# Kernel optimization log

Measured on AMD Instinct MI355X. Metric: run time of the kernel, lower is better.

## Reference

```python
import jax, jax.numpy as jnp
import numpy as np
import math

NUM_HEADS = 16
D_MODEL = 1024
HEAD_DIM = D_MODEL // NUM_HEADS


def setup_inputs() -> dict:
    key = jax.random.key(0)
    k1, k2, k3 = jax.random.split(key, 3)
    x = jax.random.normal(k1, (4, 2048, D_MODEL), dtype=jnp.float32)
    # Linear(d_model, 3*d_model, bias=False): y = x @ w_qkv, w_qkv: [d_model, 3*d_model]
    w_qkv = jax.random.normal(k2, (D_MODEL, 3 * D_MODEL), dtype=jnp.float32) * (1.0 / math.sqrt(D_MODEL))
    w_o = jax.random.normal(k3, (D_MODEL, D_MODEL), dtype=jnp.float32) * (1.0 / math.sqrt(D_MODEL))
    return {"x": x, "w_qkv": w_qkv, "w_o": w_o}


def reference(x, w_qkv, w_o):
    B, S, _ = x.shape
    H, Dh = NUM_HEADS, HEAD_DIM
    qkv = (x @ w_qkv).reshape(B, S, 3, H, Dh)
    q = qkv[:, :, 0].transpose(0, 2, 1, 3)  # [B, H, S, Dh]
    k = qkv[:, :, 1].transpose(0, 2, 1, 3)
    v = qkv[:, :, 2].transpose(0, 2, 1, 3)
    scale = 1.0 / math.sqrt(Dh + 1e-9)
    scores = jnp.einsum("bhqd,bhkd->bhqk", q, k) * scale  # [B, H, S, S]
    probs = jax.nn.softmax(scores, axis=-1)
    # dropout is identity in eval mode
    out = jnp.einsum("bhqk,bhkd->bhqd", probs, v)  # [B, H, S, Dh]
    out = out.transpose(0, 2, 1, 3).reshape(B, S, H * Dh)
    return out @ w_o
```

## Files before the change

### kernel.cpp

```cpp
#include <hip/hip_runtime.h>
#include <hip/hip_bf16.h>

typedef __bf16 bf16_t;
typedef __bf16 bf16x8 __attribute__((ext_vector_type(8)));
typedef float f32x4 __attribute__((ext_vector_type(4)));
typedef unsigned int uint32x2 __attribute__((ext_vector_type(2)));
typedef unsigned int uint32x4 __attribute__((ext_vector_type(4)));

#define B_SZ 4
#define SEQ 2048
#define NH 16
#define DH 64
#define DM 1024
#define RSQ (3 * DM)

__device__ __forceinline__ void gload_lds16(const bf16_t* g, bf16_t* l) {
  __builtin_amdgcn_global_load_lds(
      (const __attribute__((address_space(1))) unsigned int*)g,
      (__attribute__((address_space(3))) unsigned int*)l, 16, 0, 0);
}

__device__ __forceinline__ unsigned lds_b32addr(void* p) {
  return (unsigned)(uintptr_t)(__attribute__((address_space(3))) void*)p;
}

__global__ __launch_bounds__(256) void f32_to_bf16_kernel(
    const float* __restrict__ in, bf16_t* __restrict__ out, int n) {
  int i = (blockIdx.x * blockDim.x + threadIdx.x) * 4;
  if (i >= n) return;
  float4 v = *reinterpret_cast<const float4*>(in + i);
  bf16_t o[4] = {(bf16_t)v.x, (bf16_t)v.y, (bf16_t)v.z, (bf16_t)v.w};
  *reinterpret_cast<uint2*>(out + i) = *reinterpret_cast<const uint2*>(o);
}

__global__ __launch_bounds__(256) void transpose_f32_bf16_kernel(
    const float* __restrict__ in, bf16_t* __restrict__ outT, int K, int N,
    int scale_cols, float scale) {
  __shared__ float tile[32][33];
  const int tx = threadIdx.x & 31;
  const int ty = threadIdx.x >> 5;
  const int n0 = blockIdx.x * 32;
  const int k0 = blockIdx.y * 32;
#pragma unroll
  for (int j = 0; j < 4; ++j)
    tile[ty + j * 8][tx] = in[(size_t)(k0 + ty + j * 8) * N + n0 + tx];
  __syncthreads();
#pragma unroll
  for (int j = 0; j < 4; ++j) {
    int n = n0 + ty + j * 8;
    float s = (n < scale_cols) ? scale : 1.0f;
    outT[(size_t)n * K + k0 + tx] = (bf16_t)(tile[tx][ty + j * 8] * s);
  }
}

template <typename OutT>
__global__ __launch_bounds__(512, 2) void gemm_dp_kernel(
    const bf16_t* __restrict__ A, const bf16_t* __restrict__ Bt,
    OutT* __restrict__ C, int M, int N, int K, int NB) {
  __shared__ __align__(16) bf16_t As[3][128 * 64];
  __shared__ __align__(16) bf16_t Bs[3][256 * 64];

  const int tid = threadIdx.x;
  const int lane = tid & 63;
  const int wid = tid >> 6;
  const int l16 = lane & 15;
  const int g4 = lane >> 4;
  const int wm = wid >> 2;
  const int wn = wid & 3;
  const int tiles = K >> 6;

  const int nwg = gridDim.x;
  const int bid = blockIdx.x;
  const int swz = (bid & 7) * (nwg >> 3) + (bid >> 3);
  const int m0 = (swz / NB) * 128;
  const int n0 = (swz % NB) * 256;

  const int srow = tid >> 3;
  const int scol = ((tid & 7) ^ (srow & 7)) * 8;
  const bf16_t* aglob = A + (size_t)(m0 + srow) * K + scol;
  const bf16_t* bglob = Bt + (size_t)(n0 + srow) * K + scol;

  auto stage = [&](int t) {
    const int buf = t % 3;
    const int k0 = t * 64;
#pragma unroll
    for (int i = 0; i < 2; ++i)
      gload_lds16(aglob + (size_t)i * 64 * K + k0,
                  &As[buf][i * 4096 + wid * 512]);
#pragma unroll
    for (int j = 0; j < 4; ++j)
      gload_lds16(bglob + (size_t)j * 64 * K + k0,
                  &Bs[buf][j * 4096 + wid * 512]);
  };

  f32x4 acc[4][4] = {};

  stage(0);
  stage(1);
  asm volatile("s_waitcnt vmcnt(6)" ::: "memory");
  __builtin_amdgcn_s_barrier();
  __builtin_amdgcn_sched_barrier(0);

  const int xr = l16 & 7;

  for (int t = 0; t < tiles; ++t) {
    const int buf = t % 3;

    bf16x8 af[4][2], bff[4][2];
#pragma unroll
    for (int m = 0; m < 4; ++m)
#pragma unroll
      for (int ks = 0; ks < 2; ++ks)
        af[m][ks] = *reinterpret_cast<const bf16x8*>(
            &As[buf][(wm * 64 + m * 16 + l16) * 64 +
                     ((ks * 4 + g4) ^ xr) * 8]);
#pragma unroll
    for (int n = 0; n < 4; ++n)
#pragma unroll
      for (int ks = 0; ks < 2; ++ks)
        bff[n][ks] = *reinterpret_cast<const bf16x8*>(
            &Bs[buf][(wn * 64 + n * 16 + l16) * 64 +
                     ((ks * 4 + g4) ^ xr) * 8]);

    if (t + 2 < tiles) stage(t + 2);

    __builtin_amdgcn_s_setprio(1);
#pragma unroll
    for (int m = 0; m < 4; ++m)
#pragma unroll
      for (int n = 0; n < 4; ++n)
#pragma unroll
        for (int ks = 0; ks < 2; ++ks)
          acc[m][n] = __builtin_amdgcn_mfma_f32_16x16x32_bf16(
              af[m][ks], bff[n][ks], acc[m][n], 0, 0, 0);
    __builtin_amdgcn_s_setprio(0);

    if (t + 2 < tiles)
      asm volatile("s_waitcnt vmcnt(6)" ::: "memory");
    else
      asm volatile("s_waitcnt vmcnt(0)" ::: "memory");
    __builtin_amdgcn_s_barrier();
    __builtin_amdgcn_sched_barrier(0);
  }

#pragma unroll
  for (int m = 0; m < 4; ++m)
#pragma unroll
    for (int n = 0; n < 4; ++n)
#pragma unroll
      for (int r = 0; r < 4; ++r) {
        int row = m0 + wm * 64 + m * 16 + g4 * 4 + r;
        int col = n0 + wn * 64 + n * 16 + l16;
        C[(size_t)row * N + col] = (OutT)acc[m][n][r];
      }
}

template <bool PRE>
__device__ __forceinline__ void attn_body(
    const bf16_t* kp_next, const bf16_t* vp_next, bf16_t* vst_next,
    unsigned vrd, uint32x4 (&kf)[2][2], const bf16x8 (&qf)[4][2],
    const bf16x8 vones, f32x4 (&acc_o)[16], f32x4 (&acc_l)[4]) {
  if constexpr (PRE) {
#pragma unroll
    for (int t = 0; t < 4; ++t)
      gload_lds16(vp_next + t * 16, vst_next + t * 512);
  }

  if constexpr (PRE)
    asm volatile("s_waitcnt vmcnt(8)" ::: "memory");
  else
    asm volatile("s_waitcnt vmcnt(4)" ::: "memory");
  __builtin_amdgcn_sched_barrier(0);

  uint32x2 vr[4][2];
#define TRR(dst, OFFSTR)                              \
  asm volatile("ds_read_b64_tr_b16 %0, %1 offset:" OFFSTR \
               : "=v"(dst)                            \
               : "v"(vrd))
  TRR(vr[0][0], "0");    TRR(vr[0][1], "512");
  TRR(vr[1][0], "1024"); TRR(vr[1][1], "1536");
  TRR(vr[2][0], "2048"); TRR(vr[2][1], "2560");
  TRR(vr[3][0], "3072"); TRR(vr[3][1], "3584");
#undef TRR

  if constexpr (PRE)
    asm volatile("s_waitcnt vmcnt(4)" ::: "memory");
  else
    asm volatile("s_waitcnt vmcnt(0)" ::: "memory");
  __builtin_amdgcn_sched_barrier(0);

  f32x4 sA[4] = {}, sB[4] = {};
#pragma unroll
  for (int qb = 0; qb < 4; ++qb) {
    sA[qb] = __builtin_amdgcn_mfma_f32_16x16x32_bf16(
        __builtin_bit_cast(bf16x8, kf[0][0]), qf[qb][0], sA[qb], 0, 0, 0);
    sA[qb] = __builtin_amdgcn_mfma_f32_16x16x32_bf16(
        __builtin_bit_cast(bf16x8, kf[0][1]), qf[qb][1], sA[qb], 0, 0, 0);
    sB[qb] = __builtin_amdgcn_mfma_f32_16x16x32_bf16(
        __builtin_bit_cast(bf16x8, kf[1][0]), qf[qb][0], sB[qb], 0, 0, 0);
    sB[qb] = __builtin_amdgcn_mfma_f32_16x16x32_bf16(
        __builtin_bit_cast(bf16x8, kf[1][1]), qf[qb][1], sB[qb], 0, 0, 0);
  }

  if constexpr (PRE) {
#pragma unroll
    for (int half = 0; half < 2; ++half)
#pragma unroll
      for (int kh = 0; kh < 2; ++kh)
        asm volatile("global_load_dwordx4 %0, %1, off"
                     : "=v"(kf[half][kh])
                     : "v"(kp_next + (size_t)half * 64 * RSQ + kh * 32)
                     : "memory");
  }

  const unsigned psel = 0x07060302u;
  bf16x8 pf[4];
#pragma unroll
  for (int qb = 0; qb < 4; ++qb) {
    unsigned b0 = __builtin_bit_cast(unsigned, __builtin_amdgcn_exp2f(sA[qb][0]));
    unsigned b1 = __builtin_bit_cast(unsigned, __builtin_amdgcn_exp2f(sA[qb][1]));
    unsigned b2 = __builtin_bit_cast(unsigned, __builtin_amdgcn_exp2f(sA[qb][2]));
    unsigned b3 = __builtin_bit_cast(unsigned, __builtin_amdgcn_exp2f(sA[qb][3]));
    unsigned b4 = __builtin_bit_cast(unsigned, __builtin_amdgcn_exp2f(sB[qb][0]));
    unsigned b5 = __builtin_bit_cast(unsigned, __builtin_amdgcn_exp2f(sB[qb][1]));
    unsigned b6 = __builtin_bit_cast(unsigned, __builtin_amdgcn_exp2f(sB[qb][2]));
    unsigned b7 = __builtin_bit_cast(unsigned, __builtin_amdgcn_exp2f(sB[qb][3]));
    unsigned u0, u1, u2, u3;
    asm("v_perm_b32 %0, %1, %2, %3" : "=v"(u0) : "v"(b1), "v"(b0), "v"(psel));
    asm("v_perm_b32 %0, %1, %2, %3" : "=v"(u1) : "v"(b3), "v"(b2), "v"(psel));
    asm("v_perm_b32 %0, %1, %2, %3" : "=v"(u2) : "v"(b5), "v"(b4), "v"(psel));
    asm("v_perm_b32 %0, %1, %2, %3" : "=v"(u3) : "v"(b7), "v"(b6), "v"(psel));
    uint32x4 pu = {u0, u1, u2, u3};
    pf[qb] = __builtin_bit_cast(bf16x8, pu);
  }

  asm volatile("s_waitcnt lgkmcnt(0)" ::: "memory");
  __builtin_amdgcn_sched_barrier(0);
  bf16x8 vf[4];
#pragma unroll
  for (int db = 0; db < 4; ++db) {
    uint32x4 c = {vr[db][0].x, vr[db][0].y, vr[db][1].x, vr[db][1].y};
    vf[db] = __builtin_bit_cast(bf16x8, c);
  }
#pragma unroll
  for (int qb = 0; qb < 4; ++qb) {
    acc_l[qb] = __builtin_amdgcn_mfma_f32_16x16x32_bf16(
        pf[qb], vones, acc_l[qb], 0, 0, 0);
#pragma unroll
    for (int db = 0; db < 4; ++db)
      acc_o[qb * 4 + db] = __builtin_amdgcn_mfma_f32_16x16x32_bf16(
          pf[qb], vf[db], acc_o[qb * 4 + db], 0, 0, 0);
  }
}

__global__ __launch_bounds__(256) void attn_kernel(
    const bf16_t* __restrict__ qkv, bf16_t* __restrict__ out) {
  __shared__ __align__(16) unsigned char smem[33792];
  bf16_t* Vlds = (bf16_t*)smem;
  float(*Obuf)[66] = (float(*)[66])smem;
  float* lbuf = (float*)(smem + 32768);

  const int tid = threadIdx.x;
  const int lane = tid & 63;
  const int wid = tid >> 6;
  const int l16 = lane & 15;
  const int g4 = lane >> 4;

  const int D = blockIdx.x;
  const int g = ((D >> 8) << 3) + (D & 7);
  const int h = g & 15;
  const int b = g >> 4;
  const int q0 = ((D >> 3) & 31) * 64;

  const size_t base = (size_t)b * SEQ * RSQ;

  bf16x8 qf[4][2];
#pragma unroll
  for (int qb = 0; qb < 4; ++qb)
#pragma unroll
    for (int kh = 0; kh < 2; ++kh)
      qf[qb][kh] = __builtin_bit_cast(
          bf16x8, *reinterpret_cast<const uint4*>(
                      qkv + base + (size_t)(q0 + qb * 16 + l16) * RSQ + h * DH +
                      kh * 32 + g4 * 8));

  const bf16_t* kbase =
      qkv + base + (size_t)(wid * 16 + l16) * RSQ + DM + h * DH + g4 * 8;

  const int keyoff = ((lane >> 5) << 6) + wid * 16 + (((lane >> 3) & 3) << 2) +
                     ((lane >> 1) & 3);
  const bf16_t* vsrc =
      qkv + base + (size_t)keyoff * RSQ + 2 * DM + h * DH + (lane & 1) * 8;
  bf16_t* vwave = Vlds + wid * 4096;
  const unsigned vlane = lds_b32addr(vwave) + (lane << 3);

  bf16x8 vones;
#pragma unroll
  for (int e = 0; e < 8; ++e) vones[e] = (bf16_t)1.0f;

  f32x4 acc_o[16] = {};
  f32x4 acc_l[4] = {};
  uint32x4 kf[2][2];

#pragma unroll
  for (int t = 0; t < 4; ++t) gload_lds16(vsrc + t * 16, vwave + t * 512);
#pragma unroll
  for (int half = 0; half < 2; ++half)
#pragma unroll
    for (int kh = 0; kh < 2; ++kh)
      asm volatile("global_load_dwordx4 %0, %1, off"
                   : "=v"(kf[half][kh])
                   : "v"(kbase + (size_t)half * 64 * RSQ + kh * 32)
                   : "memory");

  for (int i = 0; i < 15; ++i) {
    attn_body<true>(kbase + (size_t)(i + 1) * 128 * RSQ,
                    vsrc + (size_t)(i + 1) * 128 * RSQ,
                    vwave + ((i + 1) & 1) * 2048, vlane + (i & 1) * 4096, kf,
                    qf, vones, acc_o, acc_l);
  }
  attn_body<false>(nullptr, nullptr, nullptr, vlane + 4096, kf, qf, vones,
                   acc_o, acc_l);

  if (l16 == 0) {
#pragma unroll
    for (int qb = 0; qb < 4; ++qb)
#pragma unroll
      for (int r = 0; r < 4; ++r)
        lbuf[wid * 64 + qb * 16 + g4 * 4 + r] = acc_l[qb][r];
  }

  for (int ph = 0; ph < 4; ++ph) {
    __syncthreads();
    if (wid == ph) {
#pragma unroll
      for (int qb = 0; qb < 4; ++qb)
#pragma unroll
        for (int db = 0; db < 4; ++db)
#pragma unroll
          for (int r = 0; r < 4; ++r) {
            int q = qb * 16 + g4 * 4 + r;
            int d = db * 16 + l16;
            if (ph == 0)
              Obuf[q][d] = acc_o[qb * 4 + db][r];
            else
              Obuf[q][d] += acc_o[qb * 4 + db][r];
          }
    }
  }
  __syncthreads();

  {
    int q = wid * 16 + l16;
    float l = lbuf[0 * 64 + q] + lbuf[1 * 64 + q] + lbuf[2 * 64 + q] +
              lbuf[3 * 64 + q];
    float inv = 1.f / l;
    bf16_t ob[16];
#pragma unroll
    for (int c = 0; c < 16; ++c)
      ob[c] = (bf16_t)(Obuf[q][g4 * 16 + c] * inv);
    bf16_t* op = out + (size_t)(b * SEQ + q0 + q) * DM + h * DH + g4 * 16;
    *reinterpret_cast<uint4*>(op) = *reinterpret_cast<const uint4*>(&ob[0]);
    *reinterpret_cast<uint4*>(op + 8) = *reinterpret_cast<const uint4*>(&ob[8]);
  }
}

extern "C" void kernel_launch(void* const* d_in, const int* in_sizes, int n_in,
                              void* d_out, int out_size, void* d_ws, size_t ws_size,
                              hipStream_t stream) {
  const float* x = (const float*)d_in[0];
  const float* w_qkv = (const float*)d_in[1];
  const float* w_o = (const float*)d_in[2];
  float* out = (float*)d_out;

  bf16_t* xb = (bf16_t*)d_ws;
  bf16_t* wqkvt = xb + (size_t)8192 * 1024;
  bf16_t* wot = wqkvt + (size_t)3072 * 1024;
  bf16_t* qkv = wot + (size_t)1024 * 1024;
  bf16_t* attn = qkv + (size_t)8192 * 3072;

  const float c_exp2 = 0.18033688011112042f;

  f32_to_bf16_kernel<<<8192, 256, 0, stream>>>(x, xb, 8192 * 1024);
  transpose_f32_bf16_kernel<<<dim3(3072 / 32, 1024 / 32), 256, 0, stream>>>(
      w_qkv, wqkvt, 1024, 3072, 1024, c_exp2);
  transpose_f32_bf16_kernel<<<dim3(1024 / 32, 1024 / 32), 256, 0, stream>>>(
      w_o, wot, 1024, 1024, 0, 1.0f);

  gemm_dp_kernel<bf16_t><<<768, 512, 0, stream>>>(
      xb, wqkvt, qkv, 8192, 3072, 1024, 12);
  attn_kernel<<<2048, 256, 0, stream>>>(qkv, attn);
  gemm_dp_kernel<float><<<256, 512, 0, stream>>>(
      attn, wot, out, 8192, 1024, 1024, 4);
}
```

Measured before the change: 219.6 us.

## Fuse input prep kernels and interleave GEMM loads with per-column MFMA phases

The three preprocessing launches (x conversion and the two weight transposes) become one kernel that dispatches on block index, saving two launches. The GEMM main loop is split into four phases, one per B column fragment. Each phase reads its B fragment from LDS, issues part of the next tile's global-to-LDS loads, then runs its MFMAs, with barriers and setprio around each phase to interleave memory and compute across waves. This adds many more barriers per k-tile, and that synchronisation overhead could offset the overlap gained.

```diff
diff --git a/kernel.cpp b/kernel.cpp
--- a/kernel.cpp
+++ b/kernel.cpp
@@ -24,23 +24,33 @@
   return (unsigned)(uintptr_t)(__attribute__((address_space(3))) void*)p;
 }
 
-__global__ __launch_bounds__(256) void f32_to_bf16_kernel(
-    const float* __restrict__ in, bf16_t* __restrict__ out, int n) {
-  int i = (blockIdx.x * blockDim.x + threadIdx.x) * 4;
-  if (i >= n) return;
-  float4 v = *reinterpret_cast<const float4*>(in + i);
-  bf16_t o[4] = {(bf16_t)v.x, (bf16_t)v.y, (bf16_t)v.z, (bf16_t)v.w};
-  *reinterpret_cast<uint2*>(out + i) = *reinterpret_cast<const uint2*>(o);
-}
-
-__global__ __launch_bounds__(256) void transpose_f32_bf16_kernel(
-    const float* __restrict__ in, bf16_t* __restrict__ outT, int K, int N,
-    int scale_cols, float scale) {
+__global__ __launch_bounds__(256) void prep_kernel(
+    const float* __restrict__ x, bf16_t* __restrict__ xb,
+    const float* __restrict__ w_qkv, bf16_t* __restrict__ wqkvt,
+    const float* __restrict__ w_o, bf16_t* __restrict__ wot, float qscale) {
   __shared__ float tile[32][33];
+  const int bid = blockIdx.x;
+  if (bid < 8192) {
+    int i = (bid * 256 + threadIdx.x) * 4;
+    float4 v = *reinterpret_cast<const float4*>(x + i);
+    bf16_t o[4] = {(bf16_t)v.x, (bf16_t)v.y, (bf16_t)v.z, (bf16_t)v.w};
+    *reinterpret_cast<uint2*>(xb + i) = *reinterpret_cast<const uint2*>(o);
+    return;
+  }
+  const float* in;
+  bf16_t* outT;
+  int K = 1024, N, n0, k0, scale_cols;
+  if (bid < 8192 + 3072) {
+    int i = bid - 8192;
+    in = w_qkv; outT = wqkvt; N = 3072;
+    n0 = (i % 96) * 32; k0 = (i / 96) * 32; scale_cols = 1024;
+  } else {
+    int i = bid - 8192 - 3072;
+    in = w_o; outT = wot; N = 1024;
+    n0 = (i % 32) * 32; k0 = (i / 32) * 32; scale_cols = 0;
+  }
   const int tx = threadIdx.x & 31;
   const int ty = threadIdx.x >> 5;
-  const int n0 = blockIdx.x * 32;
-  const int k0 = blockIdx.y * 32;
 #pragma unroll
   for (int j = 0; j < 4; ++j)
     tile[ty + j * 8][tx] = in[(size_t)(k0 + ty + j * 8) * N + n0 + tx];
@@ -48,7 +58,7 @@
 #pragma unroll
   for (int j = 0; j < 4; ++j) {
     int n = n0 + ty + j * 8;
-    float s = (n < scale_cols) ? scale : 1.0f;
+    float s = (n < scale_cols) ? qscale : 1.0f;
     outT[(size_t)n * K + k0 + tx] = (bf16_t)(tile[tx][ty + j * 8] * s);
   }
 }
@@ -80,7 +90,7 @@
   const bf16_t* aglob = A + (size_t)(m0 + srow) * K + scol;
   const bf16_t* bglob = Bt + (size_t)(n0 + srow) * K + scol;
 
-  auto stage = [&](int t) {
+  auto stage_all = [&](int t) {
     const int buf = t % 3;
     const int k0 = t * 64;
 #pragma unroll
@@ -95,8 +105,8 @@
 
   f32x4 acc[4][4] = {};
 
-  stage(0);
-  stage(1);
+  stage_all(0);
+  stage_all(1);
   asm volatile("s_waitcnt vmcnt(6)" ::: "memory");
   __builtin_amdgcn_s_barrier();
   __builtin_amdgcn_sched_barrier(0);
@@ -105,40 +115,108 @@
 
   for (int t = 0; t < tiles; ++t) {
     const int buf = t % 3;
-
-    bf16x8 af[4][2], bff[4][2];
+    const bool pre = (t + 2 < tiles);
+    const int pbuf = (t + 2) % 3;
+    const int pk0 = (t + 2) * 64;
+    const int abase = (wm * 64 + l16) * 64;
+    const int bbase = (wn * 64 + l16) * 64;
+
+    bf16x8 af[4][2], bf0[2], bf1[2], bf2[2], bf3[2];
+
 #pragma unroll
     for (int m = 0; m < 4; ++m)
 #pragma unroll
       for (int ks = 0; ks < 2; ++ks)
         af[m][ks] = *reinterpret_cast<const bf16x8*>(
-            &As[buf][(wm * 64 + m * 16 + l16) * 64 +
-                     ((ks * 4 + g4) ^ xr) * 8]);
-#pragma unroll
-    for (int n = 0; n < 4; ++n)
+            &As[buf][abase + m * 16 * 64 + (((ks * 4 + g4) ^ xr) * 8)]);
+#pragma unroll
+    for (int ks = 0; ks < 2; ++ks)
+      bf0[ks] = *reinterpret_cast<const bf16x8*>(
+          &Bs[buf][bbase + 0 * 16 * 64 + (((ks * 4 + g4) ^ xr) * 8)]);
+    if (pre) {
+#pragma unroll
+      for (int i = 0; i < 2; ++i)
+        gload_lds16(aglob + (size_t)i * 64 * K + pk0,
+                    &As[pbuf][i * 4096 + wid * 512]);
+    }
+    __builtin_amdgcn_s_barrier();
+    asm volatile("s_waitcnt lgkmcnt(0)" ::: "memory");
+    __builtin_amdgcn_sched_barrier(0);
+    __builtin_amdgcn_s_setprio(1);
+#pragma unroll
+    for (int m = 0; m < 4; ++m)
 #pragma unroll
       for (int ks = 0; ks < 2; ++ks)
-        bff[n][ks] = *reinterpret_cast<const bf16x8*>(
-            &Bs[buf][(wn * 64 + n * 16 + l16) * 64 +
-                     ((ks * 4 + g4) ^ xr) * 8]);
-
-    if (t + 2 < tiles) stage(t + 2);
-
+        acc[m][0] = __builtin_amdgcn_mfma_f32_16x16x32_bf16(
+            af[m][ks], bf0[ks], acc[m][0], 0, 0, 0);
+    __builtin_amdgcn_s_setprio(0);
+    __builtin_amdgcn_s_barrier();
+
+#pragma unroll
+    for (int ks = 0; ks < 2; ++ks)
+      bf1[ks] = *reinterpret_cast<const bf16x8*>(
+          &Bs[buf][bbase + 1 * 16 * 64 + (((ks * 4 + g4) ^ xr) * 8)]);
+    if (pre) {
+#pragma unroll
+      for (int j = 0; j < 2; ++j)
+        gload_lds16(bglob + (size_t)j * 64 * K + pk0,
+                    &Bs[pbuf][j * 4096 + wid * 512]);
+    }
+    __builtin_amdgcn_s_barrier();
+    asm volatile("s_waitcnt lgkmcnt(0)" ::: "memory");
+    __builtin_amdgcn_sched_barrier(0);
     __builtin_amdgcn_s_setprio(1);
 #pragma unroll
     for (int m = 0; m < 4; ++m)
 #pragma unroll
-      for (int n = 0; n < 4; ++n)
-#pragma unroll
-        for (int ks = 0; ks < 2; ++ks)
-          acc[m][n] = __builtin_amdgcn_mfma_f32_16x16x32_bf16(
-              af[m][ks], bff[n][ks], acc[m][n], 0, 0, 0);
+      for (int ks = 0; ks < 2; ++ks)
+        acc[m][1] = __builtin_amdgcn_mfma_f32_16x16x32_bf16(
+            af[m][ks], bf1[ks], acc[m][1], 0, 0, 0);
     __builtin_amdgcn_s_setprio(0);
-
-    if (t + 2 < tiles)
+    __builtin_amdgcn_s_barrier();
+
+#pragma unroll
+    for (int ks = 0; ks < 2; ++ks)
+      bf2[ks] = *reinterpret_cast<const bf16x8*>(
+          &Bs[buf][bbase + 2 * 16 * 64 + (((ks * 4 + g4) ^ xr) * 8)]);
+    if (pre) {
+#pragma unroll
+      for (int j = 2; j < 4; ++j)
+        gload_lds16(bglob + (size_t)j * 64 * K + pk0,
+                    &Bs[pbuf][j * 4096 + wid * 512]);
+    }
+    __builtin_amdgcn_s_barrier();
+    asm volatile("s_waitcnt lgkmcnt(0)" ::: "memory");
+    __builtin_amdgcn_sched_barrier(0);
+    __builtin_amdgcn_s_setprio(1);
+#pragma unroll
+    for (int m = 0; m < 4; ++m)
+#pragma unroll
+      for (int ks = 0; ks < 2; ++ks)
+        acc[m][2] = __builtin_amdgcn_mfma_f32_16x16x32_bf16(
+            af[m][ks], bf2[ks], acc[m][2], 0, 0, 0);
+    __builtin_amdgcn_s_setprio(0);
+    __builtin_amdgcn_s_barrier();
+
+#pragma unroll
+    for (int ks = 0; ks < 2; ++ks)
+      bf3[ks] = *reinterpret_cast<const bf16x8*>(
+          &Bs[buf][bbase + 3 * 16 * 64 + (((ks * 4 + g4) ^ xr) * 8)]);
+    if (pre)
       asm volatile("s_waitcnt vmcnt(6)" ::: "memory");
     else
       asm volatile("s_waitcnt vmcnt(0)" ::: "memory");
+    __builtin_amdgcn_s_barrier();
+    asm volatile("s_waitcnt lgkmcnt(0)" ::: "memory");
+    __builtin_amdgcn_sched_barrier(0);
+    __builtin_amdgcn_s_setprio(1);
+#pragma unroll
+    for (int m = 0; m < 4; ++m)
+#pragma unroll
+      for (int ks = 0; ks < 2; ++ks)
+        acc[m][3] = __builtin_amdgcn_mfma_f32_16x16x32_bf16(
+            af[m][ks], bf3[ks], acc[m][3], 0, 0, 0);
+    __builtin_amdgcn_s_setprio(0);
     __builtin_amdgcn_s_barrier();
     __builtin_amdgcn_sched_barrier(0);
   }
@@ -381,11 +459,8 @@
 
   const float c_exp2 = 0.18033688011112042f;
 
-  f32_to_bf16_kernel<<<8192, 256, 0, stream>>>(x, xb, 8192 * 1024);
-  transpose_f32_bf16_kernel<<<dim3(3072 / 32, 1024 / 32), 256, 0, stream>>>(
-      w_qkv, wqkvt, 1024, 3072, 1024, c_exp2);
-  transpose_f32_bf16_kernel<<<dim3(1024 / 32, 1024 / 32), 256, 0, stream>>>(
-      w_o, wot, 1024, 1024, 0, 1.0f);
+  prep_kernel<<<12288, 256, 0, stream>>>(x, xb, w_qkv, wqkvt, w_o, wot,
+                                         c_exp2);
 
   gemm_dp_kernel<bf16_t><<<768, 512, 0, stream>>>(
       xb, wqkvt, qkv, 8192, 3072, 1024, 12);
```

New measurement: 235.2 us. 1.07x slower.
